# Kernel tuning notes

Measured on AMD Instinct MI355X. Metric: run time of the kernel, lower is better.

## Reference

```python
import jax, jax.numpy as jnp
import numpy as np


def setup_inputs() -> dict:
    key = jax.random.key(0)
    k1, k2 = jax.random.split(key)
    N, C, V, D = 200000, 10, 2, 256
    y = jax.random.randint(k1, (N, C), 0, 2, dtype=jnp.int32)
    train_views = jax.random.normal(k2, (V, N, D), dtype=jnp.float32)
    return {"y": y, "train_views": train_views}


def reference(y, train_views):
    # Original torch code: for each view, for each class i, zero out rows where
    # y[:, i] == 1 (keep only where mask == 0), sum over nodes -> [D], and
    # concatenate across classes -> [C*D]. This is a masked per-class sum:
    #   out[v, i, d] = sum_n (y[n, i] == 0) * x[v, n, d]
    keep = (y == 0).astype(train_views.dtype)          # [N, C]
    out = jnp.einsum('nc,vnd->vcd', keep, train_views) # [V, C, D]
    V, C, D = out.shape
    return out.reshape(V, C * D)                       # concat of per-class sums
```

## Files before the change

### kernel.cpp

```cpp
#include <hip/hip_runtime.h>
#include <cstdint>

#define CCLS 10
#define DDIM 256
#define NCHUNK 512

typedef float f32x4 __attribute__((ext_vector_type(4)));

__device__ inline f32x4 ntload4(const f32x4* p) {
    return __builtin_nontemporal_load(p);
}
__device__ inline uint32_t rfl(uint32_t x) {
    return (uint32_t)__builtin_amdgcn_readfirstlane((int)x);
}

__global__ void pack_mask_kernel(const int* __restrict__ y, uint32_t* __restrict__ km, int N) {
    __shared__ int sy[256 * CCLS];
    const int base = blockIdx.x * 256;
    const int total = N * CCLS;
    for (int i = threadIdx.x; i < 256 * CCLS; i += 256) {
        int idx = base * CCLS + i;
        sy[i] = (idx < total) ? y[idx] : 1;
    }
    __syncthreads();
    const int n = base + threadIdx.x;
    if (n < N) {
        uint32_t m = 0;
        #pragma unroll
        for (int c = 0; c < CCLS; ++c)
            m |= (sy[threadIdx.x * CCLS + c] == 0 ? 1u : 0u) << c;
        km[n] = m;
    }
}

template <int EPI>
__global__ __launch_bounds__(256, 4) void masked_sum_kernel(
    const float* __restrict__ x,
    const uint32_t* __restrict__ km,
    const int* __restrict__ y,
    float* __restrict__ dst,
    int N, int rows_per_chunk, int nchunk)
{
    const int v = blockIdx.y;
    const int chunk = blockIdx.x;
    const int n0 = chunk * rows_per_chunk;
    const int n1 = min(n0 + rows_per_chunk, N);
    const int row = threadIdx.x >> 6;
    const int d4  = threadIdx.x & 63;

    f32x4 acc[CCLS];
    #pragma unroll
    for (int c = 0; c < CCLS; ++c) acc[c] = (f32x4){0.f, 0.f, 0.f, 0.f};

    const f32x4* __restrict__ xb =
        reinterpret_cast<const f32x4*>(x + (size_t)v * N * DDIM);

    auto inline_mask = [&](int n) -> uint32_t {
        uint32_t m = 0;
        #pragma unroll
        for (int c = 0; c < CCLS; ++c)
            m |= (y[n * CCLS + c] == 0 ? 1u : 0u) << c;
        return m;
    };

    int n = n0 + row;
    for (; n + 12 < n1; n += 16) {
        f32x4 x0 = ntload4(xb + (size_t)(n)      * (DDIM / 4) + d4);
        f32x4 x1 = ntload4(xb + (size_t)(n + 4)  * (DDIM / 4) + d4);
        f32x4 x2 = ntload4(xb + (size_t)(n + 8)  * (DDIM / 4) + d4);
        f32x4 x3 = ntload4(xb + (size_t)(n + 12) * (DDIM / 4) + d4);
        uint32_t m0, m1, m2, m3;
        if (EPI == 0) { m0 = km[n]; m1 = km[n + 4]; m2 = km[n + 8]; m3 = km[n + 12]; }
        else { m0 = inline_mask(n); m1 = inline_mask(n + 4); m2 = inline_mask(n + 8); m3 = inline_mask(n + 12); }
        m0 = rfl(m0); m1 = rfl(m1); m2 = rfl(m2); m3 = rfl(m3);
        #pragma unroll
        for (int c = 0; c < CCLS; ++c)
            acc[c] += (((m0 >> c) & 1u) ? 1.0f : 0.0f) * x0;
        #pragma unroll
        for (int c = 0; c < CCLS; ++c)
            acc[c] += (((m1 >> c) & 1u) ? 1.0f : 0.0f) * x1;
        #pragma unroll
        for (int c = 0; c < CCLS; ++c)
            acc[c] += (((m2 >> c) & 1u) ? 1.0f : 0.0f) * x2;
        #pragma unroll
        for (int c = 0; c < CCLS; ++c)
            acc[c] += (((m3 >> c) & 1u) ? 1.0f : 0.0f) * x3;
    }
    for (; n < n1; n += 4) {
        f32x4 x0 = ntload4(xb + (size_t)n * (DDIM / 4) + d4);
        uint32_t m0 = (EPI == 0) ? km[n] : inline_mask(n);
        m0 = rfl(m0);
        #pragma unroll
        for (int c = 0; c < CCLS; ++c)
            acc[c] += (((m0 >> c) & 1u) ? 1.0f : 0.0f) * x0;
    }

    __shared__ f32x4 lred[4][CCLS][DDIM / 4];
    #pragma unroll
    for (int c = 0; c < CCLS; ++c)
        lred[row][c][d4] = acc[c];
    __syncthreads();

    const f32x4* __restrict__ lf = &lred[0][0][0];
    if (EPI == 0) {
        f32x4* __restrict__ dstv = reinterpret_cast<f32x4*>(
            dst + ((size_t)v * nchunk + chunk) * (CCLS * DDIM));
        for (int j = threadIdx.x; j < CCLS * DDIM / 4; j += 256) {
            f32x4 s = (lf[j] + lf[640 + j]) + (lf[1280 + j] + lf[1920 + j]);
            dstv[j] = s;
        }
    } else {
        float* __restrict__ outv = dst + (size_t)v * (CCLS * DDIM);
        for (int j = threadIdx.x; j < CCLS * DDIM / 4; j += 256) {
            f32x4 s = (lf[j] + lf[640 + j]) + (lf[1280 + j] + lf[1920 + j]);
            atomicAdd(&outv[4 * j + 0], s.x);
            atomicAdd(&outv[4 * j + 1], s.y);
            atomicAdd(&outv[4 * j + 2], s.z);
            atomicAdd(&outv[4 * j + 3], s.w);
        }
    }
}

__global__ __launch_bounds__(256) void reduce_parts_kernel(
    const float* __restrict__ part, float* __restrict__ out, int nchunk)
{
    const int v = blockIdx.y, g = blockIdx.z;
    const int w = threadIdx.x >> 6, l = threadIdx.x & 63;
    const int i4 = blockIdx.x * 64 + l;
    const f32x4* __restrict__ b =
        reinterpret_cast<const f32x4*>(part + (size_t)v * nchunk * (CCLS * DDIM));
    const int cpg = nchunk / 8;
    const int p0 = g * cpg + w * (cpg / 4);
    f32x4 s0 = {0.f,0.f,0.f,0.f}, s1 = s0, s2 = s0, s3 = s0;
    #pragma unroll
    for (int k = 0; k < cpg / 4; k += 4) {
        s0 += b[(size_t)(p0 + k + 0) * (CCLS * DDIM / 4) + i4];
        s1 += b[(size_t)(p0 + k + 1) * (CCLS * DDIM / 4) + i4];
        s2 += b[(size_t)(p0 + k + 2) * (CCLS * DDIM / 4) + i4];
        s3 += b[(size_t)(p0 + k + 3) * (CCLS * DDIM / 4) + i4];
    }
    f32x4 s = (s0 + s1) + (s2 + s3);
    __shared__ f32x4 lred[4][64];
    lred[w][l] = s;
    __syncthreads();
    if (w == 0) {
        f32x4 t = (lred[0][l] + lred[1][l]) + (lred[2][l] + lred[3][l]);
        float* o = out + (size_t)v * (CCLS * DDIM) + (size_t)i4 * 4;
        atomicAdd(o + 0, t.x);
        atomicAdd(o + 1, t.y);
        atomicAdd(o + 2, t.z);
        atomicAdd(o + 3, t.w);
    }
}

extern "C" void kernel_launch(void* const* d_in, const int* in_sizes, int n_in,
                              void* d_out, int out_size, void* d_ws, size_t ws_size,
                              hipStream_t stream) {
    const int*   y = (const int*)d_in[0];
    const float* x = (const float*)d_in[1];
    float* out = (float*)d_out;

    const int N = in_sizes[0] / CCLS;
    const int V = in_sizes[1] / (N * DDIM);

    const size_t km_bytes   = ((size_t)N * sizeof(uint32_t) + 255) & ~(size_t)255;
    const size_t part_bytes = (size_t)V * NCHUNK * CCLS * DDIM * sizeof(float);

    const int rpc = (N + NCHUNK - 1) / NCHUNK;
    dim3 grid(NCHUNK, V);

    hipMemsetAsync(d_out, 0, (size_t)out_size * sizeof(float), stream);

    if (ws_size >= km_bytes + part_bytes) {
        uint32_t* km = (uint32_t*)d_ws;
        float* part = (float*)((char*)d_ws + km_bytes);
        pack_mask_kernel<<<(N + 255) / 256, 256, 0, stream>>>(y, km, N);
        masked_sum_kernel<0><<<grid, 256, 0, stream>>>(x, km, y, part, N, rpc, NCHUNK);
        reduce_parts_kernel<<<dim3(CCLS * DDIM / 256, V, 8), 256, 0, stream>>>(part, out, NCHUNK);
    } else {
        masked_sum_kernel<2><<<grid, 256, 0, stream>>>(x, nullptr, y, out, N, rpc, NCHUNK);
    }
}
```

Baseline: 83.57 us.

## Halve chunk count, deepen load unroll, and rewrite partial reduction without atomics

Cuts the number of row chunks from 512 to 256 and unrolls the row loop eight deep, so each block issues more independent streaming loads and writes fewer partial results. The reduction kernel is rewritten so that one block owns four output columns. Lanes stride over chunks and are combined with wave shuffles and a small shared-memory step, then the result is written directly. This removes the output memset and the atomics. The costs are fewer blocks in flight (512 across both views), higher register pressure from the eight-deep unroll, and a reduction grid of 160 blocks per view.

After: 78.05 us. 1.07x faster.

```diff
diff --git a/kernel.cpp b/kernel.cpp
--- a/kernel.cpp
+++ b/kernel.cpp
@@ -3,7 +3,8 @@
 
 #define CCLS 10
 #define DDIM 256
-#define NCHUNK 512
+#define NCHUNK 256
+#define UNR 8
 
 typedef float f32x4 __attribute__((ext_vector_type(4)));
 
@@ -64,35 +65,29 @@
     };
 
     int n = n0 + row;
-    for (; n + 12 < n1; n += 16) {
-        f32x4 x0 = ntload4(xb + (size_t)(n)      * (DDIM / 4) + d4);
-        f32x4 x1 = ntload4(xb + (size_t)(n + 4)  * (DDIM / 4) + d4);
-        f32x4 x2 = ntload4(xb + (size_t)(n + 8)  * (DDIM / 4) + d4);
-        f32x4 x3 = ntload4(xb + (size_t)(n + 12) * (DDIM / 4) + d4);
-        uint32_t m0, m1, m2, m3;
-        if (EPI == 0) { m0 = km[n]; m1 = km[n + 4]; m2 = km[n + 8]; m3 = km[n + 12]; }
-        else { m0 = inline_mask(n); m1 = inline_mask(n + 4); m2 = inline_mask(n + 8); m3 = inline_mask(n + 12); }
-        m0 = rfl(m0); m1 = rfl(m1); m2 = rfl(m2); m3 = rfl(m3);
+    for (; n + 4 * (UNR - 1) < n1; n += 4 * UNR) {
+        f32x4 xv[UNR];
+        uint32_t mm[UNR];
         #pragma unroll
-        for (int c = 0; c < CCLS; ++c)
-            acc[c] += (((m0 >> c) & 1u) ? 1.0f : 0.0f) * x0;
+        for (int u = 0; u < UNR; ++u)
+            xv[u] = ntload4(xb + (size_t)(n + 4 * u) * (DDIM / 4) + d4);
         #pragma unroll
-        for (int c = 0; c < CCLS; ++c)
-            acc[c] += (((m1 >> c) & 1u) ? 1.0f : 0.0f) * x1;
+        for (int u = 0; u < UNR; ++u)
+            mm[u] = (EPI == 0) ? km[n + 4 * u] : inline_mask(n + 4 * u);
         #pragma unroll
-        for (int c = 0; c < CCLS; ++c)
-            acc[c] += (((m2 >> c) & 1u) ? 1.0f : 0.0f) * x2;
-        #pragma unroll
-        for (int c = 0; c < CCLS; ++c)
-            acc[c] += (((m3 >> c) & 1u) ? 1.0f : 0.0f) * x3;
+        for (int u = 0; u < UNR; ++u) {
+            const uint32_t m = rfl(mm[u]);
+            #pragma unroll
+            for (int c = 0; c < CCLS; ++c)
+                acc[c] += (((m >> c) & 1u) ? 1.0f : 0.0f) * xv[u];
+        }
     }
     for (; n < n1; n += 4) {
         f32x4 x0 = ntload4(xb + (size_t)n * (DDIM / 4) + d4);
-        uint32_t m0 = (EPI == 0) ? km[n] : inline_mask(n);
-        m0 = rfl(m0);
+        const uint32_t m = rfl((EPI == 0) ? km[n] : inline_mask(n));
         #pragma unroll
         for (int c = 0; c < CCLS; ++c)
-            acc[c] += (((m0 >> c) & 1u) ? 1.0f : 0.0f) * x0;
+            acc[c] += (((m >> c) & 1u) ? 1.0f : 0.0f) * x0;
     }
 
     __shared__ f32x4 lred[4][CCLS][DDIM / 4];
@@ -124,32 +119,35 @@
 __global__ __launch_bounds__(256) void reduce_parts_kernel(
     const float* __restrict__ part, float* __restrict__ out, int nchunk)
 {
-    const int v = blockIdx.y, g = blockIdx.z;
+    const int v = blockIdx.y;
     const int w = threadIdx.x >> 6, l = threadIdx.x & 63;
-    const int i4 = blockIdx.x * 64 + l;
+    const int colbase = blockIdx.x * 4;
+    const int col = colbase + (l & 3);
+    const int slot = l >> 2;
+    const int cpw = nchunk / 4;
     const f32x4* __restrict__ b =
-        reinterpret_cast<const f32x4*>(part + (size_t)v * nchunk * (CCLS * DDIM));
-    const int cpg = nchunk / 8;
-    const int p0 = g * cpg + w * (cpg / 4);
-    f32x4 s0 = {0.f,0.f,0.f,0.f}, s1 = s0, s2 = s0, s3 = s0;
+        reinterpret_cast<const f32x4*>(part) + (size_t)v * nchunk * (CCLS * DDIM / 4);
+
+    f32x4 s = (f32x4){0.f, 0.f, 0.f, 0.f};
+    #pragma unroll 4
+    for (int ch = w * cpw + slot; ch < (w + 1) * cpw; ch += 16)
+        s += b[(size_t)ch * (CCLS * DDIM / 4) + col];
+
     #pragma unroll
-    for (int k = 0; k < cpg / 4; k += 4) {
-        s0 += b[(size_t)(p0 + k + 0) * (CCLS * DDIM / 4) + i4];
-        s1 += b[(size_t)(p0 + k + 1) * (CCLS * DDIM / 4) + i4];
-        s2 += b[(size_t)(p0 + k + 2) * (CCLS * DDIM / 4) + i4];
-        s3 += b[(size_t)(p0 + k + 3) * (CCLS * DDIM / 4) + i4];
+    for (int off = 4; off < 64; off <<= 1) {
+        s.x += __shfl_xor(s.x, off);
+        s.y += __shfl_xor(s.y, off);
+        s.z += __shfl_xor(s.z, off);
+        s.w += __shfl_xor(s.w, off);
     }
-    f32x4 s = (s0 + s1) + (s2 + s3);
-    __shared__ f32x4 lred[4][64];
-    lred[w][l] = s;
+
+    __shared__ f32x4 lred[4][4];
+    if (l < 4) lred[w][l] = s;
     __syncthreads();
-    if (w == 0) {
-        f32x4 t = (lred[0][l] + lred[1][l]) + (lred[2][l] + lred[3][l]);
-        float* o = out + (size_t)v * (CCLS * DDIM) + (size_t)i4 * 4;
-        atomicAdd(o + 0, t.x);
-        atomicAdd(o + 1, t.y);
-        atomicAdd(o + 2, t.z);
-        atomicAdd(o + 3, t.w);
+    if (threadIdx.x < 4) {
+        f32x4 t = (lred[0][threadIdx.x] + lred[1][threadIdx.x]) +
+                  (lred[2][threadIdx.x] + lred[3][threadIdx.x]);
+        reinterpret_cast<f32x4*>(out)[(size_t)v * (CCLS * DDIM / 4) + colbase + threadIdx.x] = t;
     }
 }
 
@@ -169,15 +167,14 @@
     const int rpc = (N + NCHUNK - 1) / NCHUNK;
     dim3 grid(NCHUNK, V);
 
-    hipMemsetAsync(d_out, 0, (size_t)out_size * sizeof(float), stream);
-
     if (ws_size >= km_bytes + part_bytes) {
         uint32_t* km = (uint32_t*)d_ws;
         float* part = (float*)((char*)d_ws + km_bytes);
         pack_mask_kernel<<<(N + 255) / 256, 256, 0, stream>>>(y, km, N);
         masked_sum_kernel<0><<<grid, 256, 0, stream>>>(x, km, y, part, N, rpc, NCHUNK);
-        reduce_parts_kernel<<<dim3(CCLS * DDIM / 256, V, 8), 256, 0, stream>>>(part, out, NCHUNK);
+        reduce_parts_kernel<<<dim3(CCLS * DDIM / 4 / 4, V), 256, 0, stream>>>(part, out, NCHUNK);
     } else {
+        hipMemsetAsync(d_out, 0, (size_t)out_size * sizeof(float), stream);
         masked_sum_kernel<2><<<grid, 256, 0, stream>>>(x, nullptr, y, out, N, rpc, NCHUNK);
     }
 }
```
